# Kernel optimization log

Hardware: AMD Instinct MI355X
Metric: run time of the kernel (lower is better)

Reference implementation:

```python
import jax, jax.numpy as jnp
import numpy as np

B, T, D_IN, E, H = 2, 2048, 1024, 64, 16  # batch, num_tokens, input dim, emb_size(per-head), num_heads


def setup_inputs() -> dict:
    key = jax.random.key(0)
    ks = jax.random.split(key, 6)
    s = 0.02
    inp = jax.random.normal(ks[0], (B, T, D_IN), dtype=jnp.float32)
    # causal mask: 1.0 where attention is disallowed (j > i), matching `scaled_compat -= mask * 1e9`
    mask = jnp.triu(jnp.ones((T, T), dtype=jnp.float32), k=1)
    Wq = jax.random.normal(ks[1], (D_IN, E * H), dtype=jnp.float32) * s
    Wk = jax.random.normal(ks[2], (D_IN, E * H), dtype=jnp.float32) * s
    Wv = jax.random.normal(ks[3], (D_IN, E * H), dtype=jnp.float32) * s
    Wu = jax.random.normal(ks[4], (E * H, E), dtype=jnp.float32) * s
    bu = jnp.zeros((E,), dtype=jnp.float32)
    return {"inp": inp, "mask": mask, "Wq": Wq, "Wk": Wk, "Wv": Wv, "Wu": Wu, "bu": bu}


def reference(inp, mask, Wq, Wk, Wv, Wu, bu):
    b = inp.shape[0]
    q = inp @ Wq  # [B,T,E*H]
    k = inp @ Wk
    v = inp @ Wv
    # NOTE: original reshapes last dim as (E, H) -> heads on fastest axis (interleaved layout)
    q = q.reshape(b, T, E, H)
    k = k.reshape(b, T, E, H)
    v = v.reshape(b, T, E, H)
    scores = jnp.einsum("bteh,bseh->bhts", q, k) / jnp.sqrt(jnp.float32(E))  # [B,H,T,T]
    if mask is not None:
        scores = scores - mask * 1e9
    attn = jax.nn.softmax(scores, axis=-1)
    wv = jnp.einsum("bhts,bseh->bhte", attn, v)  # [B,H,T,E]
    # transpose [0,2,3,1] -> [B,T,E,H], then flatten to [B,T,E*H] (H fastest, matching original)
    wv = jnp.transpose(wv, (0, 2, 3, 1)).reshape(b, T, E * H)
    return wv @ Wu + bu  # unify Dense(emb_size), with bias
```

## Files before the change

kernel.cpp:

```cpp
#include <hip/hip_runtime.h>


typedef __bf16 bf16x8 __attribute__((ext_vector_type(8)));
typedef __bf16 bf16x4 __attribute__((ext_vector_type(4)));
typedef float f32x4 __attribute__((ext_vector_type(4)));
typedef unsigned short u16;
typedef unsigned int u32;

#define AS1 __attribute__((address_space(1)))
#define AS3 __attribute__((address_space(3)))

__device__ __forceinline__ void gll16(const void* g, void* l) {
    __builtin_amdgcn_global_load_lds((const AS1 u32*)g, (AS3 u32*)l, 16, 0, 0);
}

__device__ __forceinline__ u16 f2bf(float f) {
    __bf16 h = (__bf16)f;
    union { __bf16 h; u16 u; } v; v.h = h; return v.u;
}

#define MM 4096
#define SCALE_LOG2E 0.18033688011112042f

__global__ void prep(const float* __restrict__ in, u16* __restrict__ out,
                     const float* __restrict__ Wq, const float* __restrict__ Wk,
                     const float* __restrict__ Wv, const float* __restrict__ Wu,
                     u16* __restrict__ wqt, u16* __restrict__ wkt,
                     u16* __restrict__ wvt, u16* __restrict__ wut) {
    __shared__ float lds[32][33];
    int bid = blockIdx.x, tid = threadIdx.x;
    if (bid < 4096) {
        int i = bid * 256 + tid;
        float4 f = ((const float4*)in)[i];
        bf16x4 o;
        o[0] = (__bf16)f.x; o[1] = (__bf16)f.y; o[2] = (__bf16)f.z; o[3] = (__bf16)f.w;
        ((bf16x4*)out)[i] = o;
        return;
    }
    int bid2 = bid - 4096;
    int z = bid2 >> 10, y = (bid2 >> 5) & 31, x = bid2 & 31;
    const float* src; u16* dst; int N;
    if (z == 0)      { src = Wq; dst = wqt; N = 1024; }
    else if (z == 1) { src = Wk; dst = wkt; N = 1024; }
    else if (z == 2) { src = Wv; dst = wvt; N = 1024; }
    else             { src = Wu; dst = wut; N = 64; if (y >= 2) return; }
    int k0 = x * 32, n0 = y * 32;
    int c = tid & 31, r0 = tid >> 5;
#pragma unroll
    for (int p = 0; p < 4; ++p) {
        int r = r0 + p * 8;
        lds[r][c] = src[(k0 + r) * N + n0 + c];
    }
    __syncthreads();
#pragma unroll
    for (int p = 0; p < 4; ++p) {
        int n = n0 + r0 + p * 8;
        if (z < 3) {
            int rnew = ((n & 15) << 6) | (n >> 4);
            dst[rnew * 1024 + k0 + c] = f2bf(lds[c][n - n0]);
        } else {
            int k = k0 + c;
            int kp = ((k & 15) << 6) | (k >> 4);
            dst[n * 1024 + kp] = f2bf(lds[c][n - n0]);
        }
    }
}

__global__ __launch_bounds__(256) void gemm_qkv(const u16* __restrict__ xb,
                                                const u16* __restrict__ wqt,
                                                const u16* __restrict__ wkt,
                                                const u16* __restrict__ wvt,
                                                u16* __restrict__ qh, u16* __restrict__ kh,
                                                u16* __restrict__ vh) {
    int z = blockIdx.z;
    const u16* wt = (z == 0) ? wqt : (z == 1) ? wkt : wvt;
    u16* dst      = (z == 0) ? qh  : (z == 1) ? kh  : vh;
    __shared__ u16 lA[3][128 * 32];
    __shared__ u16 lB[3][128 * 32];
    int tid = threadIdx.x;
    int m0 = blockIdx.x * 128, n0 = blockIdx.y * 128;
    int lane = tid & 63, w = tid >> 6;
    int wr = w >> 1, wc = w & 1;
    int l15 = lane & 15, quad = lane >> 4;
    f32x4 acc[4][4] = {};
    int srow = tid >> 2, scol = (tid & 3) * 8;
    const u16* ga = xb + (m0 + srow) * 1024 + scol;
    const u16* gb = wt + (n0 + srow) * 1024 + scol;
#pragma unroll
    for (int t0 = 0; t0 < 2; ++t0)
#pragma unroll
        for (int pp = 0; pp < 2; ++pp) {
            gll16(ga + pp * 65536 + t0 * 32, lA[t0] + (pp * 256 + tid) * 8);
            gll16(gb + pp * 65536 + t0 * 32, lB[t0] + (pp * 256 + tid) * 8);
        }
    int cur = 0;
#pragma unroll 1
    for (int kk = 0; kk < 32; ++kk) {
        if (kk < 31) asm volatile("s_waitcnt vmcnt(4)" ::: "memory");
        else         asm volatile("s_waitcnt vmcnt(0)" ::: "memory");
        __builtin_amdgcn_s_barrier();
        if (kk + 2 < 32) {
            int nxt = cur + 2; if (nxt >= 3) nxt -= 3;
            int kb = (kk + 2) * 32;
#pragma unroll
            for (int pp = 0; pp < 2; ++pp) {
                gll16(ga + pp * 65536 + kb, lA[nxt] + (pp * 256 + tid) * 8);
                gll16(gb + pp * 65536 + kb, lB[nxt] + (pp * 256 + tid) * 8);
            }
        }
        bf16x8 af[4], bfr[4];
#pragma unroll
        for (int i = 0; i < 4; ++i)
            af[i] = *(const bf16x8*)(lA[cur] + (wr * 64 + i * 16 + l15) * 32 + quad * 8);
#pragma unroll
        for (int j = 0; j < 4; ++j)
            bfr[j] = *(const bf16x8*)(lB[cur] + (wc * 64 + j * 16 + l15) * 32 + quad * 8);
#pragma unroll
        for (int i = 0; i < 4; ++i)
#pragma unroll
            for (int j = 0; j < 4; ++j)
                acc[i][j] = __builtin_amdgcn_mfma_f32_16x16x32_bf16(af[i], bfr[j], acc[i][j], 0, 0, 0);
        ++cur; if (cur == 3) cur = 0;
    }
    int bb = m0 >> 11;
    int hb = (n0 >> 6) + wc;
    if (z < 2) {
        float scale = (z == 0) ? SCALE_LOG2E : 1.f;
#pragma unroll
        for (int i = 0; i < 4; ++i)
#pragma unroll
            for (int r = 0; r < 4; ++r) {
                int m = m0 + wr * 64 + i * 16 + quad * 4 + r;
                bf16x4 o;
                o[0] = (__bf16)(acc[i][0][r] * scale); o[1] = (__bf16)(acc[i][1][r] * scale);
                o[2] = (__bf16)(acc[i][2][r] * scale); o[3] = (__bf16)(acc[i][3][r] * scale);
                *(bf16x4*)(dst + m * 1024 + hb * 64 + l15 * 4) = o;
            }
    } else {
#pragma unroll
        for (int j = 0; j < 4; ++j)
#pragma unroll
            for (int r = 0; r < 4; ++r) {
                bf16x4 o;
                o[0] = (__bf16)acc[0][j][r]; o[1] = (__bf16)acc[1][j][r];
                o[2] = (__bf16)acc[2][j][r]; o[3] = (__bf16)acc[3][j][r];
                *(bf16x4*)(dst + (((bb * 16 + hb) * 64) + j * 16 + l15) * 2048 +
                           (m0 & 2047) + wr * 64 + (quad * 4 + r) * 4) = o;
            }
    }
}

__global__ __launch_bounds__(256) void attn(const u16* __restrict__ qh, const u16* __restrict__ kh,
                                            const u16* __restrict__ vh, u16* __restrict__ ot,
                                            float* __restrict__ part, float* __restrict__ lp) {
    __shared__ u16 smem[25600];
    u16* sPQ = smem;
    const int tid = threadIdx.x;
    const int lane = tid & 63, w = tid >> 6;
    const int quad = lane >> 4, l15 = lane & 15;
    const int s = blockIdx.x, by = blockIdx.y;
    int qt, j0, j1, half;
    if (s < 8)       { qt = 7 - s;  j0 = 0;      j1 = 2 * qt + 2; half = -1; }
    else if (s < 16) { qt = s;      j0 = 0;      j1 = qt + 1;     half = 0;  }
    else             { qt = s - 8;  j0 = qt + 1; j1 = 2 * qt + 2; half = 1;  }
    const int b = by >> 4, h = by & 15;
    const int row0 = tid >> 3;
    const int cb0 = (tid & 7) ^ (row0 & 7);
    const u16* kg0 = kh + (b * 2048) * 1024 + h * 64 + row0 * 1024 + cb0 * 8;
    const u16* vg0 = vh + (by * 64) * 2048 + row0 * 2048 + cb0 * 8;
    const int fsw = (l15 & 7) * 8;

    const u16* qg = qh + (b * 2048 + qt * 128) * 1024 + h * 64;
#pragma unroll
    for (int p = 0; p < 4; ++p) {
        int c = p * 256 + tid;
        gll16(qg + (c >> 3) * 1024 + (c & 7) * 8, sPQ + c * 8);
    }
    __syncthreads();
    bf16x8 aq[2][2];
#pragma unroll
    for (int rg = 0; rg < 2; ++rg)
#pragma unroll
        for (int k2 = 0; k2 < 2; ++k2)
            aq[rg][k2] = *(const bf16x8*)(sPQ + (w * 32 + rg * 16 + l15) * 64 + k2 * 32 + quad * 8);

    {
        u16* sK0 = smem + 9216;
        u16* sV0 = smem + 17408;
        gll16(kg0 + j0 * 65536,         sK0 + tid * 8);
        gll16(kg0 + j0 * 65536 + 32768, sK0 + (256 + tid) * 8);
        gll16(vg0 + j0 * 64,            sV0 + tid * 8);
        gll16(vg0 + j0 * 64 + 65536,    sV0 + (256 + tid) * 8);
    }
    float lpart[2][4] = {};
    f32x4 oacc[2][4] = {};
    u16* sPw = sPQ + w * 2304;
    for (int jt = j0; jt < j1; ++jt) {
        int cur = (jt - j0) & 1;
        u16* sK = smem + 9216 + cur * 4096;
        u16* sV = smem + 17408 + cur * 4096;
        asm volatile("s_waitcnt vmcnt(0)" ::: "memory");
        __builtin_amdgcn_s_barrier();
        if (jt + 1 < j1) {
            u16* sKn = smem + 9216 + (cur ^ 1) * 4096;
            u16* sVn = smem + 17408 + (cur ^ 1) * 4096;
            gll16(kg0 + (jt + 1) * 65536,         sKn + tid * 8);
            gll16(kg0 + (jt + 1) * 65536 + 32768, sKn + (256 + tid) * 8);
            gll16(vg0 + (jt + 1) * 64,            sVn + tid * 8);
            gll16(vg0 + (jt + 1) * 64 + 65536,    sVn + (256 + tid) * 8);
        }
        f32x4 sacc[2][4] = {};
        __builtin_amdgcn_s_setprio(1);
#pragma unroll
        for (int j4 = 0; j4 < 4; ++j4)
#pragma unroll
            for (int k2 = 0; k2 < 2; ++k2) {
                bf16x8 bk = *(const bf16x8*)(sK + (j4 * 16 + l15) * 64 + (((k2 * 4 + quad) * 8) ^ fsw));
                sacc[0][j4] = __builtin_amdgcn_mfma_f32_16x16x32_bf16(aq[0][k2], bk, sacc[0][j4], 0, 0, 0);
                sacc[1][j4] = __builtin_amdgcn_mfma_f32_16x16x32_bf16(aq[1][k2], bk, sacc[1][j4], 0, 0, 0);
            }
        __builtin_amdgcn_s_setprio(0);
        if (jt >= 2 * qt) {
            int soff = (jt - 2 * qt) * 64;
#pragma unroll
            for (int rg = 0; rg < 2; ++rg)
#pragma unroll
                for (int j4 = 0; j4 < 4; ++j4)
#pragma unroll
                    for (int r = 0; r < 4; ++r) {
                        int sg = soff + j4 * 16 + l15;
                        int tg = w * 32 + rg * 16 + quad * 4 + r;
                        if (sg > tg) sacc[rg][j4][r] = -1e30f;
                    }
        }
#pragma unroll
        for (int rg = 0; rg < 2; ++rg)
#pragma unroll
            for (int r = 0; r < 4; ++r) {
                float p0 = __builtin_amdgcn_exp2f(sacc[rg][0][r]);
                float p1 = __builtin_amdgcn_exp2f(sacc[rg][1][r]);
                float p2 = __builtin_amdgcn_exp2f(sacc[rg][2][r]);
                float p3 = __builtin_amdgcn_exp2f(sacc[rg][3][r]);
                lpart[rg][r] += (p0 + p1) + (p2 + p3);
                bf16x4 o;
                o[0] = (__bf16)p0; o[1] = (__bf16)p1; o[2] = (__bf16)p2; o[3] = (__bf16)p3;
                *(bf16x4*)(sPw + (rg * 16 + quad * 4 + r) * 72 + l15 * 4) = o;
            }
        bf16x8 ap[2][2];
#pragma unroll
        for (int rg = 0; rg < 2; ++rg)
#pragma unroll
            for (int k2 = 0; k2 < 2; ++k2)
                ap[rg][k2] = *(const bf16x8*)(sPw + (rg * 16 + l15) * 72 + k2 * 32 + quad * 8);
        __builtin_amdgcn_s_setprio(1);
#pragma unroll
        for (int e4 = 0; e4 < 4; ++e4)
#pragma unroll
            for (int k2 = 0; k2 < 2; ++k2) {
                bf16x8 bv = *(const bf16x8*)(sV + (e4 * 16 + l15) * 64 + (((k2 * 4 + quad) * 8) ^ fsw));
                oacc[0][e4] = __builtin_amdgcn_mfma_f32_16x16x32_bf16(ap[0][k2], bv, oacc[0][e4], 0, 0, 0);
                oacc[1][e4] = __builtin_amdgcn_mfma_f32_16x16x32_bf16(ap[1][k2], bv, oacc[1][e4], 0, 0, 0);
            }
        __builtin_amdgcn_s_setprio(0);
    }
    if (half < 0) {
#pragma unroll
        for (int rg = 0; rg < 2; ++rg)
#pragma unroll
            for (int r = 0; r < 4; ++r) {
                float rs = lpart[rg][r];
#pragma unroll
                for (int off = 1; off < 16; off <<= 1) rs += __shfl_xor(rs, off, 16);
                float inv = 1.f / rs;
                int t = qt * 128 + w * 32 + rg * 16 + quad * 4 + r;
                int base = (b * 2048 + t) * 1024 + h * 64;
#pragma unroll
                for (int e4 = 0; e4 < 4; ++e4)
                    ot[base + e4 * 16 + l15] = f2bf(oacc[rg][e4][r] * inv);
            }
    } else {
        int pb = by * 8 + (qt - 8);
        float* pg = part + (pb * 2 + half) * 8192;
        float* lg = lp + pb * 256 + half * 128;
#pragma unroll
        for (int rg = 0; rg < 2; ++rg)
#pragma unroll
            for (int r = 0; r < 4; ++r) {
                float rs = lpart[rg][r];
#pragma unroll
                for (int off = 1; off < 16; off <<= 1) rs += __shfl_xor(rs, off, 16);
                int row = w * 32 + rg * 16 + quad * 4 + r;
                if (l15 == 0) lg[row] = rs;
#pragma unroll
                for (int e4 = 0; e4 < 4; ++e4)
                    pg[row * 64 + e4 * 16 + l15] = oacc[rg][e4][r];
            }
    }
}

__global__ __launch_bounds__(256) void gemm_out(const u16* __restrict__ ot,
                                                const float* __restrict__ part,
                                                const float* __restrict__ lp,
                                                const u16* __restrict__ wut,
                                                const float* __restrict__ bu, float* __restrict__ out) {
    __shared__ float red[4][1088];
    int tid = threadIdx.x, lane = tid & 63, w = tid >> 6;
    int quad = lane >> 4, l15 = lane & 15;
    int m0 = blockIdx.x * 16;
    int b = m0 >> 11, t0 = m0 & 2047, qt = t0 >> 7;
    f32x4 acc[4] = {};
    const u16* bptr = wut + l15 * 1024 + w * 256 + quad * 8;
    if (qt < 8) {
        const u16* aptr = ot + (m0 + l15) * 1024 + w * 256 + quad * 8;
#pragma unroll
        for (int kk = 0; kk < 8; ++kk) {
            bf16x8 af = *(const bf16x8*)(aptr + kk * 32);
#pragma unroll
            for (int j = 0; j < 4; ++j) {
                bf16x8 bfr = *(const bf16x8*)(bptr + j * 16 * 1024 + kk * 32);
                acc[j] = __builtin_amdgcn_mfma_f32_16x16x32_bf16(af, bfr, acc[j], 0, 0, 0);
            }
        }
    } else {
        int rowp = (t0 & 127) + l15;
        float inv4[4];
#pragma unroll
        for (int hh = 0; hh < 4; ++hh) {
            int pb = (b * 16 + w * 4 + hh) * 8 + (qt - 8);
            inv4[hh] = 1.f / (lp[pb * 256 + rowp] + lp[pb * 256 + 128 + rowp]);
        }
#pragma unroll
        for (int kk = 0; kk < 8; ++kk) {
            const int hh = kk >> 1;
            int pb = (b * 16 + w * 4 + hh) * 8 + (qt - 8);
            int e = (kk & 1) * 32 + quad * 8;
            const float* pA = part + pb * 16384 + rowp * 64 + e;
            float4 a0 = *(const float4*)(pA);
            float4 a1 = *(const float4*)(pA + 4);
            float4 c0 = *(const float4*)(pA + 8192);
            float4 c1 = *(const float4*)(pA + 8192 + 4);
            float inv = inv4[hh];
            bf16x8 af;
            af[0] = (__bf16)((a0.x + c0.x) * inv); af[1] = (__bf16)((a0.y + c0.y) * inv);
            af[2] = (__bf16)((a0.z + c0.z) * inv); af[3] = (__bf16)((a0.w + c0.w) * inv);
            af[4] = (__bf16)((a1.x + c1.x) * inv); af[5] = (__bf16)((a1.y + c1.y) * inv);
            af[6] = (__bf16)((a1.z + c1.z) * inv); af[7] = (__bf16)((a1.w + c1.w) * inv);
#pragma unroll
            for (int j = 0; j < 4; ++j) {
                bf16x8 bfr = *(const bf16x8*)(bptr + j * 16 * 1024 + kk * 32);
                acc[j] = __builtin_amdgcn_mfma_f32_16x16x32_bf16(af, bfr, acc[j], 0, 0, 0);
            }
        }
    }
#pragma unroll
    for (int j = 0; j < 4; ++j)
#pragma unroll
        for (int r = 0; r < 4; ++r)
            red[w][(j * 16 + l15) * 17 + quad * 4 + r] = acc[j][r];
    __syncthreads();
    int n = tid & 63, mq = tid >> 6;
    float bias = bu[n];
#pragma unroll
    for (int i = 0; i < 4; ++i) {
        int m = mq * 4 + i;
        float s = red[0][n * 17 + m] + red[1][n * 17 + m] + red[2][n * 17 + m] + red[3][n * 17 + m];
        out[(m0 + m) * 64 + n] = s + bias;
    }
}

#define OFF_XB   0u
#define OFF_WQT  8388608u
#define OFF_WKT  10485760u
#define OFF_WVT  12582912u
#define OFF_WUT  14680064u
#define OFF_QH   14811136u
#define OFF_KH   23199744u
#define OFF_VH   31588352u
#define OFF_OT   OFF_XB
#define OFF_PART 39976960u
#define OFF_LP   56754176u

extern "C" void kernel_launch(void* const* d_in, const int* in_sizes, int n_in,
                              void* d_out, int out_size, void* d_ws, size_t ws_size,
                              hipStream_t stream) {
    (void)in_sizes; (void)n_in; (void)out_size; (void)ws_size;
    const float* inp = (const float*)d_in[0];
    const float* Wq = (const float*)d_in[2];
    const float* Wk = (const float*)d_in[3];
    const float* Wv = (const float*)d_in[4];
    const float* Wu = (const float*)d_in[5];
    const float* bu = (const float*)d_in[6];
    float* out = (float*)d_out;
    char* ws = (char*)d_ws;
    u16* xb  = (u16*)(ws + OFF_XB);
    u16* wqt = (u16*)(ws + OFF_WQT);
    u16* wkt = (u16*)(ws + OFF_WKT);
    u16* wvt = (u16*)(ws + OFF_WVT);
    u16* wut = (u16*)(ws + OFF_WUT);
    u16* qh  = (u16*)(ws + OFF_QH);
    u16* kh  = (u16*)(ws + OFF_KH);
    u16* vh  = (u16*)(ws + OFF_VH);
    u16* ot  = (u16*)(ws + OFF_OT);
    float* part = (float*)(ws + OFF_PART);
    float* lpw  = (float*)(ws + OFF_LP);

    prep<<<8192, 256, 0, stream>>>(inp, xb, Wq, Wk, Wv, Wu, wqt, wkt, wvt, wut);
    gemm_qkv<<<dim3(32, 8, 3), 256, 0, stream>>>(xb, wqt, wkt, wvt, qh, kh, vh);
    attn<<<dim3(24, 32), 256, 0, stream>>>(qh, kh, vh, ot, part, lpw);
    gemm_out<<<256, 256, 0, stream>>>(ot, part, lpw, wut, bu, out);
}
```

Measured before the change: 160.8 us.

## Compute S transposed so P stays in registers as MFMA A operand

Swaps the MFMA operand order for QK^T so each lane holds a full row of scores. This lets the exponentiated probabilities be packed straight into the A-operand registers for the PV MFMA, removing the per-wave LDS round trip for P. The V projection store is permuted so the V layout matches the new P k-ordering, the causal mask indices are transposed, and the row-sum reduction becomes a cross-quad shuffle. LDS use drops, and the change relies on consistent index permutations across three kernels.

```diff
diff --git a/kernel.cpp b/kernel.cpp
--- a/kernel.cpp
+++ b/kernel.cpp
@@ -145,7 +145,7 @@
                 o[0] = (__bf16)acc[0][j][r]; o[1] = (__bf16)acc[1][j][r];
                 o[2] = (__bf16)acc[2][j][r]; o[3] = (__bf16)acc[3][j][r];
                 *(bf16x4*)(dst + (((bb * 16 + hb) * 64) + j * 16 + l15) * 2048 +
-                           (m0 & 2047) + wr * 64 + (quad * 4 + r) * 4) = o;
+                           (m0 & 2047) + wr * 64 + (r >> 1) * 32 + quad * 8 + (r & 1) * 4) = o;
             }
     }
 }
@@ -153,8 +153,8 @@
 __global__ __launch_bounds__(256) void attn(const u16* __restrict__ qh, const u16* __restrict__ kh,
                                             const u16* __restrict__ vh, u16* __restrict__ ot,
                                             float* __restrict__ part, float* __restrict__ lp) {
-    __shared__ u16 smem[25600];
-    u16* sPQ = smem;
+    __shared__ u16 smem[24576];
+    u16* sQ = smem;
     const int tid = threadIdx.x;
     const int lane = tid & 63, w = tid >> 6;
     const int quad = lane >> 4, l15 = lane & 15;
@@ -174,7 +174,7 @@
 #pragma unroll
     for (int p = 0; p < 4; ++p) {
         int c = p * 256 + tid;
-        gll16(qg + (c >> 3) * 1024 + (c & 7) * 8, sPQ + c * 8);
+        gll16(qg + (c >> 3) * 1024 + (c & 7) * 8, sQ + c * 8);
     }
     __syncthreads();
     bf16x8 aq[2][2];
@@ -182,28 +182,27 @@
     for (int rg = 0; rg < 2; ++rg)
 #pragma unroll
         for (int k2 = 0; k2 < 2; ++k2)
-            aq[rg][k2] = *(const bf16x8*)(sPQ + (w * 32 + rg * 16 + l15) * 64 + k2 * 32 + quad * 8);
+            aq[rg][k2] = *(const bf16x8*)(sQ + (w * 32 + rg * 16 + l15) * 64 + k2 * 32 + quad * 8);
 
     {
-        u16* sK0 = smem + 9216;
-        u16* sV0 = smem + 17408;
+        u16* sK0 = smem + 8192;
+        u16* sV0 = smem + 16384;
         gll16(kg0 + j0 * 65536,         sK0 + tid * 8);
         gll16(kg0 + j0 * 65536 + 32768, sK0 + (256 + tid) * 8);
         gll16(vg0 + j0 * 64,            sV0 + tid * 8);
         gll16(vg0 + j0 * 64 + 65536,    sV0 + (256 + tid) * 8);
     }
-    float lpart[2][4] = {};
+    float lpart[2] = {0.f, 0.f};
     f32x4 oacc[2][4] = {};
-    u16* sPw = sPQ + w * 2304;
     for (int jt = j0; jt < j1; ++jt) {
         int cur = (jt - j0) & 1;
-        u16* sK = smem + 9216 + cur * 4096;
-        u16* sV = smem + 17408 + cur * 4096;
+        u16* sK = smem + 8192 + cur * 4096;
+        u16* sV = smem + 16384 + cur * 4096;
         asm volatile("s_waitcnt vmcnt(0)" ::: "memory");
         __builtin_amdgcn_s_barrier();
         if (jt + 1 < j1) {
-            u16* sKn = smem + 9216 + (cur ^ 1) * 4096;
-            u16* sVn = smem + 17408 + (cur ^ 1) * 4096;
+            u16* sKn = smem + 8192 + (cur ^ 1) * 4096;
+            u16* sVn = smem + 16384 + (cur ^ 1) * 4096;
             gll16(kg0 + (jt + 1) * 65536,         sKn + tid * 8);
             gll16(kg0 + (jt + 1) * 65536 + 32768, sKn + (256 + tid) * 8);
             gll16(vg0 + (jt + 1) * 64,            sVn + tid * 8);
@@ -216,8 +215,8 @@
 #pragma unroll
             for (int k2 = 0; k2 < 2; ++k2) {
                 bf16x8 bk = *(const bf16x8*)(sK + (j4 * 16 + l15) * 64 + (((k2 * 4 + quad) * 8) ^ fsw));
-                sacc[0][j4] = __builtin_amdgcn_mfma_f32_16x16x32_bf16(aq[0][k2], bk, sacc[0][j4], 0, 0, 0);
-                sacc[1][j4] = __builtin_amdgcn_mfma_f32_16x16x32_bf16(aq[1][k2], bk, sacc[1][j4], 0, 0, 0);
+                sacc[0][j4] = __builtin_amdgcn_mfma_f32_16x16x32_bf16(bk, aq[0][k2], sacc[0][j4], 0, 0, 0);
+                sacc[1][j4] = __builtin_amdgcn_mfma_f32_16x16x32_bf16(bk, aq[1][k2], sacc[1][j4], 0, 0, 0);
             }
         __builtin_amdgcn_s_setprio(0);
         if (jt >= 2 * qt) {
@@ -228,30 +227,28 @@
                 for (int j4 = 0; j4 < 4; ++j4)
 #pragma unroll
                     for (int r = 0; r < 4; ++r) {
-                        int sg = soff + j4 * 16 + l15;
-                        int tg = w * 32 + rg * 16 + quad * 4 + r;
+                        int sg = soff + j4 * 16 + quad * 4 + r;
+                        int tg = w * 32 + rg * 16 + l15;
                         if (sg > tg) sacc[rg][j4][r] = -1e30f;
                     }
         }
-#pragma unroll
-        for (int rg = 0; rg < 2; ++rg)
-#pragma unroll
-            for (int r = 0; r < 4; ++r) {
-                float p0 = __builtin_amdgcn_exp2f(sacc[rg][0][r]);
-                float p1 = __builtin_amdgcn_exp2f(sacc[rg][1][r]);
-                float p2 = __builtin_amdgcn_exp2f(sacc[rg][2][r]);
-                float p3 = __builtin_amdgcn_exp2f(sacc[rg][3][r]);
-                lpart[rg][r] += (p0 + p1) + (p2 + p3);
-                bf16x4 o;
-                o[0] = (__bf16)p0; o[1] = (__bf16)p1; o[2] = (__bf16)p2; o[3] = (__bf16)p3;
-                *(bf16x4*)(sPw + (rg * 16 + quad * 4 + r) * 72 + l15 * 4) = o;
-            }
         bf16x8 ap[2][2];
 #pragma unroll
-        for (int rg = 0; rg < 2; ++rg)
+        for (int rg = 0; rg < 2; ++rg) {
+            float pe[4][4];
+#pragma unroll
+            for (int j4 = 0; j4 < 4; ++j4) {
+#pragma unroll
+                for (int r = 0; r < 4; ++r)
+                    pe[j4][r] = __builtin_amdgcn_exp2f(sacc[rg][j4][r]);
+                lpart[rg] += (pe[j4][0] + pe[j4][1]) + (pe[j4][2] + pe[j4][3]);
+            }
 #pragma unroll
             for (int k2 = 0; k2 < 2; ++k2)
-                ap[rg][k2] = *(const bf16x8*)(sPw + (rg * 16 + l15) * 72 + k2 * 32 + quad * 8);
+#pragma unroll
+                for (int ip = 0; ip < 8; ++ip)
+                    ap[rg][k2][ip] = (__bf16)pe[ip & 3][k2 * 2 + (ip >> 2)];
+        }
         __builtin_amdgcn_s_setprio(1);
 #pragma unroll
         for (int e4 = 0; e4 < 4; ++e4)
@@ -265,36 +262,38 @@
     }
     if (half < 0) {
 #pragma unroll
-        for (int rg = 0; rg < 2; ++rg)
+        for (int rg = 0; rg < 2; ++rg) {
+            float tot = lpart[rg];
+            tot += __shfl_xor(tot, 16, 64);
+            tot += __shfl_xor(tot, 32, 64);
 #pragma unroll
             for (int r = 0; r < 4; ++r) {
-                float rs = lpart[rg][r];
-#pragma unroll
-                for (int off = 1; off < 16; off <<= 1) rs += __shfl_xor(rs, off, 16);
-                float inv = 1.f / rs;
+                float inv = 1.f / __shfl(tot, quad * 4 + r, 16);
                 int t = qt * 128 + w * 32 + rg * 16 + quad * 4 + r;
                 int base = (b * 2048 + t) * 1024 + h * 64;
 #pragma unroll
                 for (int e4 = 0; e4 < 4; ++e4)
                     ot[base + e4 * 16 + l15] = f2bf(oacc[rg][e4][r] * inv);
             }
+        }
     } else {
         int pb = by * 8 + (qt - 8);
         float* pg = part + (pb * 2 + half) * 8192;
         float* lg = lp + pb * 256 + half * 128;
 #pragma unroll
-        for (int rg = 0; rg < 2; ++rg)
+        for (int rg = 0; rg < 2; ++rg) {
+            float tot = lpart[rg];
+            tot += __shfl_xor(tot, 16, 64);
+            tot += __shfl_xor(tot, 32, 64);
+            if (quad == 0) lg[w * 32 + rg * 16 + l15] = tot;
 #pragma unroll
             for (int r = 0; r < 4; ++r) {
-                float rs = lpart[rg][r];
-#pragma unroll
-                for (int off = 1; off < 16; off <<= 1) rs += __shfl_xor(rs, off, 16);
                 int row = w * 32 + rg * 16 + quad * 4 + r;
-                if (l15 == 0) lg[row] = rs;
 #pragma unroll
                 for (int e4 = 0; e4 < 4; ++e4)
                     pg[row * 64 + e4 * 16 + l15] = oacc[rg][e4][r];
             }
+        }
     }
 }
 
```

Measured after the change: 160.5 us. Within noise of the previous version (-0.1%).
